# Performance work log

Measured on AMD Instinct MI355X. Metric: run time of the kernel, lower is better.

Reference implementation:

```python
import jax, jax.numpy as jnp
import numpy as np

H, D = 20, 64  # n_head, head_dim (n_state = 1280)


def setup_inputs() -> dict:
    key = jax.random.key(0)
    ks = jax.random.split(key, 14)
    B, S, N, R = 2, 1500, 1280, 32
    s = 0.05  # keep activations/scores numerically tame
    return {
        "x":   jax.random.normal(ks[0], (B, S, N), jnp.float32),
        "Wq1": jax.random.normal(ks[1], (R, N), jnp.float32) * s,
        "Wq2": jax.random.normal(ks[2], (N, R), jnp.float32) * s,
        "bq":  jax.random.normal(ks[3], (N,), jnp.float32) * s,
        "Wk1": jax.random.normal(ks[4], (R, N), jnp.float32) * s,
        "Wk2": jax.random.normal(ks[5], (N, R), jnp.float32) * s,
        "bk":  jax.random.normal(ks[6], (N,), jnp.float32) * s,
        "Wv1": jax.random.normal(ks[7], (R, N), jnp.float32) * s,
        "Wv2": jax.random.normal(ks[8], (N, R), jnp.float32) * s,
        "bv":  jax.random.normal(ks[9], (N,), jnp.float32) * s,
        "Wo1": jax.random.normal(ks[10], (R, N), jnp.float32) * s,
        "Wo2": jax.random.normal(ks[11], (N, R), jnp.float32) * s,
        "bo":  jax.random.normal(ks[12], (N,), jnp.float32) * s,
    }


def reference(x, Wq1, Wq2, bq, Wk1, Wk2, bk, Wv1, Wv2, bv, Wo1, Wo2, bo):
    B, S, N = x.shape
    # rank-r projections (the only full-size GEMMs over x)
    q1 = x @ Wq1.T  # (B,S,rq)
    k1 = x @ Wk1.T  # (B,S,rk)
    v1 = x @ Wv1.T  # (B,S,rv)
    # per-head factors, matching prepare_custom_kernel()
    Wq2h = Wq2.reshape(H, D, -1).transpose(0, 2, 1)  # (H,rq,D)
    Wk2h = Wk2.reshape(H, D, -1)                     # (H,D,rk)
    Wv2h = Wv2.reshape(H, D, -1).transpose(0, 2, 1)  # (H,rv,D)
    Wm = Wq2h @ Wk2h                                  # (H,rq,rk)
    bqh = bq.reshape(H, 1, D)                         # (H,1,D)
    bkh = bk.reshape(H, 1, D).transpose(0, 2, 1)      # (H,D,1)
    b1 = (Wq2h @ bkh)[:, :, 0]                        # (H,rq)
    b2 = (bqh @ Wk2h)[:, 0, :]                        # (H,rk)
    b3 = (bqh @ bkh)[:, 0, 0]                         # (H,)
    # merged low-rank attention scores: (q1 Wq2 + bq)(Wk2^T k1^T + bk)
    scores = jnp.einsum('bir,hrt,bjt->bhij', q1, Wm, k1)
    scores = scores + jnp.einsum('bir,hr->bhi', q1, b1)[:, :, :, None]
    scores = scores + jnp.einsum('bjt,ht->bhj', k1, b2)[:, :, None, :]
    scores = scores + b3[None, :, None, None]
    attn = jax.nn.softmax(scores * (D ** -0.5), axis=-1)  # SDPA default scale
    Vh = jnp.einsum('bjr,hrd->bhjd', v1, Wv2h)            # (B,H,S,D)
    a = jnp.einsum('bhij,bhjd->bhid', attn, Vh)           # (B,H,S,D)
    wv = a.transpose(0, 2, 1, 3).reshape(B, S, H * D) + bv
    # out projection (also low-rank)
    return (wv @ Wo1.T) @ Wo2.T + bo
```

## Files before the change

kernel.cpp:

```cpp
#include <hip/hip_runtime.h>
#include <math.h>

#define Bb 2
#define Ss 1500
#define SP 1536
#define Nn 1280
#define Hh 20
#define Rr 32
#define NT 24

#define LOG2E 1.44269504088896f

typedef __attribute__((ext_vector_type(8))) short short8;
typedef __attribute__((ext_vector_type(4))) float f32x4;
typedef unsigned short ushort_t;

__device__ __forceinline__ unsigned short f2bf(float f) {
  unsigned u = __float_as_uint(f);
  u += 0x7fffu + ((u >> 16) & 1u);
  return (unsigned short)(u >> 16);
}
__device__ __forceinline__ float bf2f(unsigned short u) {
  return __uint_as_float((unsigned)u << 16);
}
__device__ __forceinline__ unsigned cvtpk(float a, float b) {
  unsigned d;
  asm("v_cvt_pk_bf16_f32 %0, %1, %2" : "=v"(d) : "v"(a), "v"(b));
  return d;
}
__device__ __forceinline__ float fexp2(float x) {
  float r;
  asm("v_exp_f32 %0, %1" : "=v"(r) : "v"(x));
  return r;
}

__device__ __forceinline__ void gload16(const void* g, void* l) {
  __builtin_amdgcn_global_load_lds((const __attribute__((address_space(1))) unsigned int*)g,
                                   (__attribute__((address_space(3))) unsigned int*)l, 16, 0, 0);
}
__device__ __forceinline__ void gload4(const void* g, void* l) {
  __builtin_amdgcn_global_load_lds((const __attribute__((address_space(1))) unsigned int*)g,
                                   (__attribute__((address_space(3))) unsigned int*)l, 4, 0, 0);
}

#define BAR()                                  \
  do {                                         \
    asm volatile("" ::: "memory");             \
    __builtin_amdgcn_s_barrier();              \
    asm volatile("" ::: "memory");             \
  } while (0)

#define VMW(n) asm volatile("s_waitcnt vmcnt(" #n ")" ::: "memory")


__global__ void prep_kernel(const float* __restrict__ x, const float* __restrict__ Wq1,
                            const float* __restrict__ Wk1, const float* __restrict__ Wv1,
                            const float* __restrict__ Wo1, const float* __restrict__ Wq2,
                            const float* __restrict__ Wk2, const float* __restrict__ Wv2,
                            const float* __restrict__ bq, ushort_t* __restrict__ xb,
                            ushort_t* __restrict__ wcatb, ushort_t* __restrict__ wo1b,
                            ushort_t* __restrict__ wv2b, float* __restrict__ wm,
                            float* __restrict__ b2s) {
  int bid = blockIdx.x, tid = threadIdx.x;
  __shared__ float q2s[2048], k2s[2048], bqs[64];
  if (bid < 1920) {
    int gid = bid * 256 + tid;
    int gr = gid / 160, c8 = gid % 160;
    int b = gr / SP, i = gr - b * SP;
    short8 v = (short8){0, 0, 0, 0, 0, 0, 0, 0};
    if (i < Ss) {
      const float* src = x + ((size_t)(b * Ss + i)) * 1280 + c8 * 8;
      float4 a0 = *(const float4*)src;
      float4 a1 = *(const float4*)(src + 4);
      v[0] = (short)f2bf(a0.x); v[1] = (short)f2bf(a0.y);
      v[2] = (short)f2bf(a0.z); v[3] = (short)f2bf(a0.w);
      v[4] = (short)f2bf(a1.x); v[5] = (short)f2bf(a1.y);
      v[6] = (short)f2bf(a1.z); v[7] = (short)f2bf(a1.w);
    }
    *(short8*)(xb + (size_t)gr * 1280 + c8 * 8) = v;
  } else if (bid < 2060) {
    int gid = (bid - 1920) * 256 + tid;
    const float* src = nullptr;
    ushort_t* dst = nullptr;
    if (gid < 20480) {
      int row = gid / 160, c8 = gid % 160;
      dst = wcatb + (size_t)row * 1280 + c8 * 8;
      if (row < 32) src = Wq1 + (size_t)row * 1280 + c8 * 8;
      else if (row < 64) src = Wk1 + (size_t)(row - 32) * 1280 + c8 * 8;
      else if (row < 96) src = Wv1 + (size_t)(row - 64) * 1280 + c8 * 8;
    } else if (gid < 30720) {
      int g = gid - 20480;
      int row = g / 160, c8 = g % 160;
      dst = wo1b + (size_t)row * 1280 + c8 * 8;
      if (row < 32) src = Wo1 + (size_t)row * 1280 + c8 * 8;
    } else {
      int g = gid - 30720;
      int row = g >> 2, c8 = g & 3;
      dst = wv2b + row * 32 + c8 * 8;
      src = Wv2 + row * 32 + c8 * 8;
    }
    short8 v = (short8){0, 0, 0, 0, 0, 0, 0, 0};
    if (src) {
      #pragma unroll
      for (int j = 0; j < 8; ++j) v[j] = (short)f2bf(src[j]);
    }
    *(short8*)dst = v;
  } else {
    int h = bid - 2060;
    for (int e = tid; e < 2048; e += 256) {
      q2s[e] = Wq2[h * 2048 + e];
      k2s[e] = Wk2[h * 2048 + e];
    }
    if (tid < 64) bqs[tid] = bq[h * 64 + tid];
    __syncthreads();
    for (int e = tid; e < 1024; e += 256) {
      int r = e >> 5, t = e & 31;
      float s = 0.f;
      #pragma unroll 16
      for (int d = 0; d < 64; ++d) s += q2s[d * 32 + r] * k2s[d * 32 + t];
      wm[h * 1024 + r * 32 + t] = s * (0.125f * LOG2E);
    }
    if (tid < 32) {
      float s = 0.f;
      #pragma unroll 16
      for (int d = 0; d < 64; ++d) s += bqs[d] * k2s[d * 32 + tid];
      b2s[h * 32 + tid] = s * (0.125f * LOG2E);
    }
  }
}

__global__ __launch_bounds__(128) void gemm_qkv_kernel(
    const ushort_t* __restrict__ xbg, const ushort_t* __restrict__ wcat,
    float* __restrict__ xpq, ushort_t* __restrict__ k1b, ushort_t* __restrict__ v1b) {
  int tid = threadIdx.x, w = tid >> 6, l = tid & 63, l15 = l & 15, l4 = l >> 4;
  int row0 = blockIdx.x * 32;
  __shared__ __align__(16) short As[2][2048];
  __shared__ __align__(16) short Bs[2][6144];
  int sw8 = (((l & 7) ^ ((l >> 3) & 7)) << 3);
  const ushort_t* asrc0 = xbg + (size_t)(row0 + w * 16 + (l >> 3)) * 1280 + sw8;
  const ushort_t* asrc1 = asrc0 + (size_t)8 * 1280;
  const ushort_t* bsrc[6];
  #pragma unroll
  for (int g = 0; g < 6; ++g)
    bsrc[g] = wcat + (size_t)(w * 48 + g * 8 + (l >> 3)) * 1280 + sw8;

#define QSTAGE(bufi, kk)                                            \
  do {                                                              \
    gload16(asrc0 + (kk), &As[bufi][w * 1024]);                     \
    gload16(asrc1 + (kk), &As[bufi][w * 1024 + 512]);               \
    gload16(bsrc[0] + (kk), &Bs[bufi][w * 3072]);                   \
    gload16(bsrc[1] + (kk), &Bs[bufi][w * 3072 + 512]);             \
    gload16(bsrc[2] + (kk), &Bs[bufi][w * 3072 + 1024]);            \
    gload16(bsrc[3] + (kk), &Bs[bufi][w * 3072 + 1536]);            \
    gload16(bsrc[4] + (kk), &Bs[bufi][w * 3072 + 2048]);            \
    gload16(bsrc[5] + (kk), &Bs[bufi][w * 3072 + 2560]);            \
  } while (0)

  f32x4 acc[6];
  #pragma unroll
  for (int nf = 0; nf < 6; ++nf) acc[nf] = (f32x4){0.f, 0.f, 0.f, 0.f};

  QSTAGE(0, 0);
  int cur = 0;
  for (int t = 0; t < 20; ++t) {
    if (t < 19) {
      QSTAGE(cur ^ 1, (t + 1) * 64);
      VMW(8);
    } else {
      VMW(0);
    }
    BAR();
    #pragma unroll
    for (int ks = 0; ks < 2; ++ks) {
      short8 af = *(const short8*)&As[cur][(w * 16 + l15) * 64 +
                                           (((ks * 4 + l4) ^ (l15 & 7)) << 3)];
      #pragma unroll
      for (int nf = 0; nf < 6; ++nf) {
        short8 bf = *(const short8*)&Bs[cur][(nf * 16 + l15) * 64 +
                                             (((ks * 4 + l4) ^ (l15 & 7)) << 3)];
        acc[nf] = __builtin_amdgcn_mfma_f32_16x16x32_bf16(af, bf, acc[nf], 0, 0, 0);
      }
    }
    BAR();
    cur ^= 1;
  }
#undef QSTAGE

  #pragma unroll
  for (int nf = 0; nf < 6; ++nf) {
    int o = nf * 16 + l15;
    #pragma unroll
    for (int reg = 0; reg < 4; ++reg) {
      int gr = row0 + w * 16 + l4 * 4 + reg;
      int b = (gr >= SP) ? 1 : 0;
      int i = gr - b * SP;
      if (i < Ss) {
        float v = acc[nf][reg];
        if (o < 32) xpq[((size_t)b * Ss + i) * 32 + o] = v;
        else if (o < 64) k1b[((size_t)b * SP + i) * 32 + (o - 32)] = f2bf(v);
        else v1b[((size_t)b * 32 + (o - 64)) * SP + i] = f2bf(v);
      }
    }
  }
}

__global__ void qh_kb_kernel(const float* __restrict__ xpq, const float* __restrict__ wm,
                             const float* __restrict__ b2s, const ushort_t* __restrict__ k1b,
                             ushort_t* __restrict__ qhb, float* __restrict__ kbp) {
  int tid = threadIdx.x, b = blockIdx.z;
  if (blockIdx.y == 20) {
    int j0 = blockIdx.x * 64;
    __shared__ float k1s[64 * 33];
    __shared__ float b2sh[20 * 33];
    for (int e = tid; e < 2048; e += 256) {
      int row = e >> 5, t = e & 31;
      k1s[row * 33 + t] = bf2f(k1b[((size_t)b * SP + j0 + row) * 32 + t]);
    }
    for (int e = tid; e < 640; e += 256) b2sh[(e >> 5) * 33 + (e & 31)] = b2s[e];
    __syncthreads();
    for (int e = tid; e < 1280; e += 256) {
      int h = e >> 6, rw = e & 63;
      int j = j0 + rw;
      float s = -1e30f;
      if (j < Ss) {
        s = 0.f;
        #pragma unroll 8
        for (int t = 0; t < 32; ++t) s += k1s[rw * 33 + t] * b2sh[h * 33 + t];
      }
      kbp[((size_t)b * Hh + h) * SP + j] = s;
    }
  } else {
    int it = blockIdx.x, h = blockIdx.y;
    int i0 = it * 64;
    __shared__ float q1s[64 * 33];
    __shared__ float wms[1024];
    for (int e = tid; e < 2048; e += 256) {
      int row = e >> 5, r = e & 31;
      int i = i0 + row;
      q1s[row * 33 + r] = (i < Ss) ? xpq[((size_t)b * Ss + i) * 32 + r] : 0.f;
    }
    for (int e = tid; e < 1024; e += 256) wms[e] = wm[h * 1024 + e];
    __syncthreads();
    int row = tid >> 2, tc = (tid & 3) * 8;
    float o[8];
    #pragma unroll
    for (int j = 0; j < 8; ++j) o[j] = 0.f;
    for (int r = 0; r < 32; ++r) {
      float qv = q1s[row * 33 + r];
      #pragma unroll
      for (int j = 0; j < 8; ++j) o[j] += qv * wms[r * 32 + tc + j];
    }
    short8 sv;
    #pragma unroll
    for (int j = 0; j < 8; ++j) sv[j] = (short)f2bf(o[j]);
    *(short8*)(qhb + ((size_t)(b * Hh + h) * SP + i0 + row) * 32 + tc) = sv;
  }
}

__global__ __launch_bounds__(256) void attn2_kernel(
    const ushort_t* __restrict__ qhg, const ushort_t* __restrict__ k1g,
    const ushort_t* __restrict__ v1g, const ushort_t* __restrict__ wv2g,
    const float* __restrict__ kbg, const float* __restrict__ bv, ushort_t* __restrict__ wvb) {
  int it = blockIdx.x, h = blockIdx.y, b = blockIdx.z;
  int bh = b * Hh + h;
  int i0 = it * 64;
  int tid = threadIdx.x, w = tid >> 6, l = tid & 63;
  int l15 = l & 15, l4 = l >> 4;

  __shared__ short kS[2][2048];
  __shared__ short vS[2][2048];
  __shared__ float kbS[2][64];
  __shared__ short pS[4][1024];
  __shared__ short p2S[4][512];

  short8 qa = *(const short8*)(qhg + ((size_t)bh * SP + i0 + w * 16 + l15) * 32 + l4 * 8);
  short8 wb0 = *(const short8*)(wv2g + (size_t)(h * 64 + 0 * 16 + l15) * 32 + l4 * 8);
  short8 wb1 = *(const short8*)(wv2g + (size_t)(h * 64 + 1 * 16 + l15) * 32 + l4 * 8);
  short8 wb2 = *(const short8*)(wv2g + (size_t)(h * 64 + 2 * 16 + l15) * 32 + l4 * 8);
  short8 wb3 = *(const short8*)(wv2g + (size_t)(h * 64 + 3 * 16 + l15) * 32 + l4 * 8);
  VMW(0);

  const ushort_t* ksrc = k1g + (size_t)b * SP * 32 + l * 32 + w * 8;
  const ushort_t* vsrc =
      v1g + ((size_t)b * 32 + w * 8 + (l >> 3)) * SP + (((l & 7) ^ ((l >> 3) & 7)) << 3);
  const float* kbsrc = kbg + (size_t)bh * SP + l;

#define STAGE(bufi, tt)                                   \
  do {                                                    \
    int j0s = (tt) * 64;                                  \
    gload16(ksrc + (size_t)j0s * 32, &kS[bufi][w * 512]); \
    gload16(vsrc + j0s, &vS[bufi][w * 512]);              \
    if (w == 0) gload4(kbsrc + j0s, &kbS[bufi][0]);       \
  } while (0)

  STAGE(0, 0);

  f32x4 pv1[2];
  pv1[0] = (f32x4){0.f, 0.f, 0.f, 0.f};
  pv1[1] = (f32x4){0.f, 0.f, 0.f, 0.f};
  float psr[4] = {0.f, 0.f, 0.f, 0.f};
  const f32x4 zf = (f32x4){0.f, 0.f, 0.f, 0.f};

  int cur = 0;
  for (int t = 0; t < NT; ++t) {
    if (t < NT - 1) {
      STAGE(cur ^ 1, t + 1);
      if (w == 0) VMW(3); else VMW(2);
    } else {
      VMW(0);
    }
    BAR();

    #pragma unroll
    for (int nb = 0; nb < 4; ++nb) {
      short8 kf = *(const short8*)&kS[cur][l4 * 512 + (nb * 16 + l15) * 8];
      f32x4 c = __builtin_amdgcn_mfma_f32_16x16x32_bf16(qa, kf, zf, 0, 0, 0);
      float kbv = kbS[cur][nb * 16 + l15];
      int slot_lo = nb * 2 + (l15 >> 3);
      #pragma unroll
      for (int reg = 0; reg < 4; ++reg) {
        int q = l4 * 4 + reg;
        float p = fexp2(c[reg] + kbv);
        psr[reg] += p;
        pS[w][q * 64 + ((slot_lo ^ (q & 7)) << 3) + (l15 & 7)] = (short)cvtpk(p, p);
      }
    }

    #pragma unroll
    for (int kh = 0; kh < 2; ++kh) {
      short8 pa = *(const short8*)&pS[w][l15 * 64 + (((kh * 4 + l4) ^ (l15 & 7)) << 3)];
      #pragma unroll
      for (int nf = 0; nf < 2; ++nf) {
        short8 vf =
            *(const short8*)&vS[cur][(nf * 16 + l15) * 64 + (((kh * 4 + l4) ^ (l15 & 7)) << 3)];
        pv1[nf] = __builtin_amdgcn_mfma_f32_16x16x32_bf16(pa, vf, pv1[nf], 0, 0, 0);
      }
    }

    BAR();
    cur ^= 1;
  }
#undef STAGE

  #pragma unroll
  for (int nf = 0; nf < 2; ++nf) {
    #pragma unroll
    for (int reg = 0; reg < 4; ++reg) {
      int q = l4 * 4 + reg;
      int slot = nf * 2 + (l15 >> 3);
      p2S[w][q * 32 + ((slot ^ ((q >> 1) & 3)) << 3) + (l15 & 7)] =
          (short)cvtpk(pv1[nf][reg], pv1[nf][reg]);
    }
  }
  short8 pa2 = *(const short8*)&p2S[w][l15 * 32 + ((l4 ^ ((l15 >> 1) & 3)) << 3)];

  f32x4 acc[4];
  acc[0] = __builtin_amdgcn_mfma_f32_16x16x32_bf16(pa2, wb0, zf, 0, 0, 0);
  acc[1] = __builtin_amdgcn_mfma_f32_16x16x32_bf16(pa2, wb1, zf, 0, 0, 0);
  acc[2] = __builtin_amdgcn_mfma_f32_16x16x32_bf16(pa2, wb2, zf, 0, 0, 0);
  acc[3] = __builtin_amdgcn_mfma_f32_16x16x32_bf16(pa2, wb3, zf, 0, 0, 0);

  #pragma unroll
  for (int reg = 0; reg < 4; ++reg) {
    #pragma unroll
    for (int m = 1; m < 16; m <<= 1) psr[reg] += __shfl_xor(psr[reg], m, 64);
  }
  float inv[4];
  #pragma unroll
  for (int reg = 0; reg < 4; ++reg) inv[reg] = 1.f / psr[reg];

  #pragma unroll
  for (int db = 0; db < 4; ++db) {
    float bvv = bv[h * 64 + db * 16 + l15];
    #pragma unroll
    for (int reg = 0; reg < 4; ++reg) {
      int qi = i0 + w * 16 + l4 * 4 + reg;
      if (qi < Ss)
        wvb[((size_t)(b * SP + qi)) * 1280 + h * 64 + db * 16 + l15] =
            f2bf(acc[db][reg] * inv[reg] + bvv);
    }
  }
}

__global__ __launch_bounds__(128) void gemm_o1_kernel(const ushort_t* __restrict__ wvg,
                                                      const ushort_t* __restrict__ wo1,
                                                      float* __restrict__ tbuf) {
  int tid = threadIdx.x, w = tid >> 6, l = tid & 63, l15 = l & 15, l4 = l >> 4;
  int row0 = blockIdx.x * 32;
  __shared__ __align__(16) short As[2][2048];
  __shared__ __align__(16) short Bs[2][2048];
  int sw8 = (((l & 7) ^ ((l >> 3) & 7)) << 3);
  const ushort_t* asrc0 = wvg + (size_t)(row0 + w * 16 + (l >> 3)) * 1280 + sw8;
  const ushort_t* asrc1 = asrc0 + (size_t)8 * 1280;
  const ushort_t* bsrc = wo1 + (size_t)(w * 16 + (l >> 3)) * 1280 + sw8;
  const ushort_t* bsrc1 = bsrc + (size_t)8 * 1280;

#define OSTAGE(bufi, kk)                                 \
  do {                                                   \
    gload16(asrc0 + (kk), &As[bufi][w * 1024]);          \
    gload16(asrc1 + (kk), &As[bufi][w * 1024 + 512]);    \
    gload16(bsrc + (kk), &Bs[bufi][w * 1024]);           \
    gload16(bsrc1 + (kk), &Bs[bufi][w * 1024 + 512]);    \
  } while (0)

  f32x4 acc[2];
  acc[0] = (f32x4){0.f, 0.f, 0.f, 0.f};
  acc[1] = (f32x4){0.f, 0.f, 0.f, 0.f};
  OSTAGE(0, 0);
  int cur = 0;
  for (int t = 0; t < 20; ++t) {
    if (t < 19) {
      OSTAGE(cur ^ 1, (t + 1) * 64);
      VMW(4);
    } else {
      VMW(0);
    }
    BAR();
    #pragma unroll
    for (int ks = 0; ks < 2; ++ks) {
      short8 af = *(const short8*)&As[cur][(w * 16 + l15) * 64 +
                                           (((ks * 4 + l4) ^ (l15 & 7)) << 3)];
      #pragma unroll
      for (int nf = 0; nf < 2; ++nf) {
        short8 bf = *(const short8*)&Bs[cur][(nf * 16 + l15) * 64 +
                                             (((ks * 4 + l4) ^ (l15 & 7)) << 3)];
        acc[nf] = __builtin_amdgcn_mfma_f32_16x16x32_bf16(af, bf, acc[nf], 0, 0, 0);
      }
    }
    BAR();
    cur ^= 1;
  }
#undef OSTAGE

  #pragma unroll
  for (int nf = 0; nf < 2; ++nf) {
    int o = nf * 16 + l15;
    #pragma unroll
    for (int reg = 0; reg < 4; ++reg) {
      int gr = row0 + w * 16 + l4 * 4 + reg;
      int b = (gr >= SP) ? 1 : 0;
      int i = gr - b * SP;
      if (i < Ss) tbuf[((size_t)b * Ss + i) * 32 + o] = acc[nf][reg];
    }
  }
}

__global__ void proj_o2_kernel(const float* __restrict__ tbuf, const float* __restrict__ Wo2,
                               const float* __restrict__ bo, float* __restrict__ out) {
  int rb = blockIdx.x, nb = blockIdx.y, tid = threadIdx.x;
  int rowbase = rb * 16, n0 = nb * 256;
  __shared__ float ts[16 * 33];
  __shared__ float wos[256 * 33];
  for (int e = tid; e < 8192; e += 256) {
    int nloc = e >> 5, o = e & 31;
    wos[nloc * 33 + o] = Wo2[(size_t)(n0 + nloc) * 32 + o];
  }
  for (int e = tid; e < 512; e += 256) {
    int row = e >> 5, o = e & 31;
    int gr = rowbase + row;
    ts[row * 33 + o] = (gr < Bb * Ss) ? tbuf[(size_t)gr * 32 + o] : 0.f;
  }
  __syncthreads();
  int n = n0 + tid;
  float bias = bo[n];
  for (int row = 0; row < 16; ++row) {
    int gr = rowbase + row;
    if (gr >= Bb * Ss) break;
    float s = bias;
    #pragma unroll 8
    for (int o = 0; o < 32; ++o) s += ts[row * 33 + o] * wos[tid * 33 + o];
    out[(size_t)gr * 1280 + n] = s;
  }
}

extern "C" void kernel_launch(void* const* d_in, const int* in_sizes, int n_in,
                              void* d_out, int out_size, void* d_ws, size_t ws_size,
                              hipStream_t stream) {
  const float* x   = (const float*)d_in[0];
  const float* Wq1 = (const float*)d_in[1];
  const float* Wq2 = (const float*)d_in[2];
  const float* bq  = (const float*)d_in[3];
  const float* Wk1 = (const float*)d_in[4];
  const float* Wk2 = (const float*)d_in[5];
  const float* Wv1 = (const float*)d_in[7];
  const float* Wv2 = (const float*)d_in[8];
  const float* bv  = (const float*)d_in[9];
  const float* Wo1 = (const float*)d_in[10];
  const float* Wo2 = (const float*)d_in[11];
  const float* bo  = (const float*)d_in[12];
  float* out = (float*)d_out;
  float* ws  = (float*)d_ws;

  if (ws_size < (size_t)5431424 * sizeof(float)) return;

  float* wm    = ws;
  float* b2s   = ws + 20480;
  float* xpq   = ws + 21120;
  float* kb    = ws + 117120;
  float* tbuf  = ws + 178560;
  ushort_t* qhb   = (ushort_t*)(ws + 274560);
  ushort_t* k1b   = (ushort_t*)(ws + 1257600);
  ushort_t* v1b   = (ushort_t*)(ws + 1306752);
  ushort_t* xb    = (ushort_t*)(ws + 1355904);
  ushort_t* wcatb = (ushort_t*)(ws + 3321984);
  ushort_t* wo1b  = (ushort_t*)(ws + 3403904);
  ushort_t* wv2b  = (ushort_t*)(ws + 3444864);
  ushort_t* wvb   = (ushort_t*)(ws + 3465344);

  prep_kernel<<<2080, 256, 0, stream>>>(x, Wq1, Wk1, Wv1, Wo1, Wq2, Wk2, Wv2, bq,
                                        xb, wcatb, wo1b, wv2b, wm, b2s);
  gemm_qkv_kernel<<<96, 128, 0, stream>>>(xb, wcatb, xpq, k1b, v1b);
  qh_kb_kernel<<<dim3(NT, 21, Bb), 256, 0, stream>>>(xpq, wm, b2s, k1b, qhb, kb);
  attn2_kernel<<<dim3(NT, Hh, Bb), 256, 0, stream>>>(qhb, k1b, v1b, wv2b, kb, bv, wvb);
  gemm_o1_kernel<<<96, 128, 0, stream>>>(wvb, wo1b, tbuf);
  proj_o2_kernel<<<dim3(188, 5), 256, 0, stream>>>(tbuf, Wo2, bo, out);
}
```

Baseline: 104.2 us.

## Split attention over key halves and combine partials in a separate kernel

The attention kernel now splits the key/value sequence into two halves across an extra grid dimension, doubling the block count from 960 to 1920. Each block writes fp32 partial PV accumulators and row sums to workspace. A new combine kernel sums the halves, applies the Wv2 projection in fp32 FMA, normalizes, adds the bias and writes bf16 output. This targets occupancy on the many-CU GPU, at the cost of an extra launch, about 16 MB of partial-buffer traffic, and a scalar rather than MFMA final projection. Splitting without a max-shift is only valid because the softmax here uses no max subtraction.

```diff
diff --git a/kernel.cpp b/kernel.cpp
--- a/kernel.cpp
+++ b/kernel.cpp
@@ -257,11 +257,12 @@
   }
 }
 
-__global__ __launch_bounds__(256) void attn2_kernel(
+__global__ __launch_bounds__(256) void attn_split_kernel(
     const ushort_t* __restrict__ qhg, const ushort_t* __restrict__ k1g,
-    const ushort_t* __restrict__ v1g, const ushort_t* __restrict__ wv2g,
-    const float* __restrict__ kbg, const float* __restrict__ bv, ushort_t* __restrict__ wvb) {
-  int it = blockIdx.x, h = blockIdx.y, b = blockIdx.z;
+    const ushort_t* __restrict__ v1g, const float* __restrict__ kbg,
+    float* __restrict__ pv1p, float* __restrict__ psump) {
+  int it = blockIdx.x, h = blockIdx.y, z = blockIdx.z;
+  int b = z >> 1, jh = z & 1;
   int bh = b * Hh + h;
   int i0 = it * 64;
   int tid = threadIdx.x, w = tid >> 6, l = tid & 63;
@@ -271,13 +272,8 @@
   __shared__ short vS[2][2048];
   __shared__ float kbS[2][64];
   __shared__ short pS[4][1024];
-  __shared__ short p2S[4][512];
 
   short8 qa = *(const short8*)(qhg + ((size_t)bh * SP + i0 + w * 16 + l15) * 32 + l4 * 8);
-  short8 wb0 = *(const short8*)(wv2g + (size_t)(h * 64 + 0 * 16 + l15) * 32 + l4 * 8);
-  short8 wb1 = *(const short8*)(wv2g + (size_t)(h * 64 + 1 * 16 + l15) * 32 + l4 * 8);
-  short8 wb2 = *(const short8*)(wv2g + (size_t)(h * 64 + 2 * 16 + l15) * 32 + l4 * 8);
-  short8 wb3 = *(const short8*)(wv2g + (size_t)(h * 64 + 3 * 16 + l15) * 32 + l4 * 8);
   VMW(0);
 
   const ushort_t* ksrc = k1g + (size_t)b * SP * 32 + l * 32 + w * 8;
@@ -293,7 +289,8 @@
     if (w == 0) gload4(kbsrc + j0s, &kbS[bufi][0]);       \
   } while (0)
 
-  STAGE(0, 0);
+  int base = jh * 12;
+  STAGE(0, base);
 
   f32x4 pv1[2];
   pv1[0] = (f32x4){0.f, 0.f, 0.f, 0.f};
@@ -302,9 +299,9 @@
   const f32x4 zf = (f32x4){0.f, 0.f, 0.f, 0.f};
 
   int cur = 0;
-  for (int t = 0; t < NT; ++t) {
-    if (t < NT - 1) {
-      STAGE(cur ^ 1, t + 1);
+  for (int tt = 0; tt < 12; ++tt) {
+    if (tt < 11) {
+      STAGE(cur ^ 1, base + tt + 1);
       if (w == 0) VMW(3); else VMW(2);
     } else {
       VMW(0);
@@ -343,42 +340,87 @@
 #undef STAGE
 
   #pragma unroll
+  for (int reg = 0; reg < 4; ++reg) {
+    #pragma unroll
+    for (int m = 1; m < 16; m <<= 1) psr[reg] += __shfl_xor(psr[reg], m, 64);
+  }
+
+  size_t tix = (size_t)bh * 24 + it;
+  float* pvdst = pv1p + tix * 4096 + (size_t)jh * 2048;
+  #pragma unroll
   for (int nf = 0; nf < 2; ++nf) {
     #pragma unroll
     for (int reg = 0; reg < 4; ++reg) {
-      int q = l4 * 4 + reg;
-      int slot = nf * 2 + (l15 >> 3);
-      p2S[w][q * 32 + ((slot ^ ((q >> 1) & 3)) << 3) + (l15 & 7)] =
-          (short)cvtpk(pv1[nf][reg], pv1[nf][reg]);
-    }
-  }
-  short8 pa2 = *(const short8*)&p2S[w][l15 * 32 + ((l4 ^ ((l15 >> 1) & 3)) << 3)];
-
-  f32x4 acc[4];
-  acc[0] = __builtin_amdgcn_mfma_f32_16x16x32_bf16(pa2, wb0, zf, 0, 0, 0);
-  acc[1] = __builtin_amdgcn_mfma_f32_16x16x32_bf16(pa2, wb1, zf, 0, 0, 0);
-  acc[2] = __builtin_amdgcn_mfma_f32_16x16x32_bf16(pa2, wb2, zf, 0, 0, 0);
-  acc[3] = __builtin_amdgcn_mfma_f32_16x16x32_bf16(pa2, wb3, zf, 0, 0, 0);
-
-  #pragma unroll
-  for (int reg = 0; reg < 4; ++reg) {
-    #pragma unroll
-    for (int m = 1; m < 16; m <<= 1) psr[reg] += __shfl_xor(psr[reg], m, 64);
-  }
-  float inv[4];
-  #pragma unroll
-  for (int reg = 0; reg < 4; ++reg) inv[reg] = 1.f / psr[reg];
-
-  #pragma unroll
-  for (int db = 0; db < 4; ++db) {
-    float bvv = bv[h * 64 + db * 16 + l15];
-    #pragma unroll
-    for (int reg = 0; reg < 4; ++reg) {
-      int qi = i0 + w * 16 + l4 * 4 + reg;
-      if (qi < Ss)
-        wvb[((size_t)(b * SP + qi)) * 1280 + h * 64 + db * 16 + l15] =
-            f2bf(acc[db][reg] * inv[reg] + bvv);
-    }
+      pvdst[(w * 16 + l4 * 4 + reg) * 32 + nf * 16 + l15] = pv1[nf][reg];
+    }
+  }
+  if (l15 == 0) {
+    float* pd = psump + tix * 128 + jh * 64 + w * 16 + l4 * 4;
+    #pragma unroll
+    for (int reg = 0; reg < 4; ++reg) pd[reg] = psr[reg];
+  }
+}
+
+__global__ __launch_bounds__(256) void combine_kernel(
+    const float* __restrict__ pv1p, const float* __restrict__ psump,
+    const ushort_t* __restrict__ wv2g, const float* __restrict__ bv,
+    ushort_t* __restrict__ wvb) {
+  int it = blockIdx.x, h = blockIdx.y, b = blockIdx.z;
+  size_t tix = (size_t)(b * Hh + h) * 24 + it;
+  int tid = threadIdx.x;
+  __shared__ __align__(16) float pv[64 * 36];
+  __shared__ __align__(16) float wv2f[32 * 68];
+  __shared__ float ps[64];
+
+  const float* src = pv1p + tix * 4096;
+  for (int e = tid; e < 2048; e += 256) {
+    int q = e >> 5, r = e & 31;
+    pv[q * 36 + r] = src[e] + src[2048 + e];
+  }
+  for (int e = tid; e < 2048; e += 256) {
+    int d = e >> 5, r = e & 31;
+    wv2f[r * 68 + d] = bf2f(wv2g[h * 2048 + e]);
+  }
+  if (tid < 64) ps[tid] = psump[tix * 128 + tid] + psump[tix * 128 + 64 + tid];
+  __syncthreads();
+
+  int q = tid >> 2, dg = tid & 3;
+  float pvr[32];
+  #pragma unroll
+  for (int c = 0; c < 8; ++c) {
+    float4 v = *(const float4*)&pv[q * 36 + c * 4];
+    pvr[c * 4 + 0] = v.x; pvr[c * 4 + 1] = v.y;
+    pvr[c * 4 + 2] = v.z; pvr[c * 4 + 3] = v.w;
+  }
+  float o[16];
+  #pragma unroll
+  for (int k = 0; k < 16; ++k) o[k] = 0.f;
+  #pragma unroll 8
+  for (int r = 0; r < 32; ++r) {
+    float p = pvr[r];
+    #pragma unroll
+    for (int c = 0; c < 4; ++c) {
+      float4 wv = *(const float4*)&wv2f[r * 68 + dg * 16 + c * 4];
+      o[c * 4 + 0] += p * wv.x;
+      o[c * 4 + 1] += p * wv.y;
+      o[c * 4 + 2] += p * wv.z;
+      o[c * 4 + 3] += p * wv.w;
+    }
+  }
+
+  float inv = 1.f / ps[q];
+  int qi = it * 64 + q;
+  if (qi < Ss) {
+    unsigned pk[8];
+    #pragma unroll
+    for (int m = 0; m < 8; ++m) {
+      float b0 = bv[h * 64 + dg * 16 + 2 * m];
+      float b1 = bv[h * 64 + dg * 16 + 2 * m + 1];
+      pk[m] = cvtpk(o[2 * m] * inv + b0, o[2 * m + 1] * inv + b1);
+    }
+    unsigned* dst = (unsigned*)(wvb + ((size_t)b * SP + qi) * 1280 + h * 64 + dg * 16);
+    *(uint4*)dst = make_uint4(pk[0], pk[1], pk[2], pk[3]);
+    *(uint4*)(dst + 4) = make_uint4(pk[4], pk[5], pk[6], pk[7]);
   }
 }
 
@@ -491,7 +533,7 @@
   float* out = (float*)d_out;
   float* ws  = (float*)d_ws;
 
-  if (ws_size < (size_t)5431424 * sizeof(float)) return;
+  if (ws_size < (size_t)9486464 * sizeof(float)) return;
 
   float* wm    = ws;
   float* b2s   = ws + 20480;
@@ -506,12 +548,15 @@
   ushort_t* wo1b  = (ushort_t*)(ws + 3403904);
   ushort_t* wv2b  = (ushort_t*)(ws + 3444864);
   ushort_t* wvb   = (ushort_t*)(ws + 3465344);
+  float* pv1p  = ws + 5431424;
+  float* psump = ws + 9363584;
 
   prep_kernel<<<2080, 256, 0, stream>>>(x, Wq1, Wk1, Wv1, Wo1, Wq2, Wk2, Wv2, bq,
                                         xb, wcatb, wo1b, wv2b, wm, b2s);
   gemm_qkv_kernel<<<96, 128, 0, stream>>>(xb, wcatb, xpq, k1b, v1b);
   qh_kb_kernel<<<dim3(NT, 21, Bb), 256, 0, stream>>>(xpq, wm, b2s, k1b, qhb, kb);
-  attn2_kernel<<<dim3(NT, Hh, Bb), 256, 0, stream>>>(qhb, k1b, v1b, wv2b, kb, bv, wvb);
+  attn_split_kernel<<<dim3(NT, Hh, 4), 256, 0, stream>>>(qhb, k1b, v1b, kb, pv1p, psump);
+  combine_kernel<<<dim3(NT, Hh, Bb), 256, 0, stream>>>(pv1p, psump, wv2b, bv, wvb);
   gemm_o1_kernel<<<96, 128, 0, stream>>>(wvb, wo1b, tbuf);
   proj_o2_kernel<<<dim3(188, 5), 256, 0, stream>>>(tbuf, Wo2, bo, out);
 }
```

Result: slower. 110.8 us (+6.3%).
